# Kernel tuning notes

Measured on AMD Instinct MI355X. Metric: run time of the kernel, lower is better.

## Reference

```python
import jax, jax.numpy as jnp
import numpy as np

N_NODES = 100000
N_EDGES = 3200000
D_IN = 128
D_OUT = 128


def setup_inputs() -> dict:
    key = jax.random.key(0)
    k1, k2, k3 = jax.random.split(key, 3)
    x = jax.random.normal(k1, (N_NODES, D_IN), dtype=jnp.float32)
    edge_index = jax.random.randint(k2, (2, N_EDGES), 0, N_NODES, dtype=jnp.int64)
    # Glorot-style init for GCN weight
    W = jax.random.normal(k3, (D_IN, D_OUT), dtype=jnp.float32) * (1.0 / np.sqrt(D_IN))
    b = jnp.zeros((D_OUT,), dtype=jnp.float32)
    return {"x": x, "edge_index": edge_index, "W": W, "b": b}


def reference(x, edge_index, W, b):
    # GCNConv (PyG semantics): add self-loops, symmetric normalization
    # D^-1/2 A D^-1/2, linear transform, aggregate, add bias; then ReLU.
    N = x.shape[0]
    loops = jnp.arange(N, dtype=edge_index.dtype)
    row = jnp.concatenate([edge_index[0], loops])  # source nodes
    col = jnp.concatenate([edge_index[1], loops])  # target nodes
    # degree over targets, with self-loop weight 1
    deg = jax.ops.segment_sum(jnp.ones_like(col, dtype=x.dtype), col,
                              num_segments=N)
    dinv = jnp.where(deg > 0, 1.0 / jnp.sqrt(deg), 0.0)
    norm = dinv[row] * dinv[col]                   # [E+N]
    xl = x @ W                                     # [N, D_OUT] dense GEMM
    msgs = xl[row] * norm[:, None]                 # gather + scale  [E+N, D_OUT]
    agg = jax.ops.segment_sum(msgs, col, num_segments=N)  # scatter-add
    return jax.nn.relu(agg + b)
```

## Files before the change

### kernel.cpp

```cpp
#include <hip/hip_runtime.h>
#include <hip/hip_bf16.h>
#include <math.h>

#define DF 128
#define TILE_EDGES 6144
#define NPB 128
#define BSH 7
#define NB_MAX 1024
#define KP 136
#define CAP 4864

typedef __hip_bfloat16 bf16;
typedef __attribute__((ext_vector_type(8))) short short8;
typedef __attribute__((ext_vector_type(4))) float f32x4;

__device__ inline short bf16bits(float f) {
    __hip_bfloat16 h = __float2bfloat16(f);
    return *reinterpret_cast<short*>(&h);
}

__device__ inline float4 unpack4(float2 p) {
    unsigned u0 = __float_as_uint(p.x), u1 = __float_as_uint(p.y);
    float4 r;
    r.x = __uint_as_float(u0 << 16);
    r.y = __uint_as_float(u0 & 0xffff0000u);
    r.z = __uint_as_float(u1 << 16);
    r.w = __uint_as_float(u1 & 0xffff0000u);
    return r;
}

__global__ __launch_bounds__(512) void k_binc(const int* __restrict__ col,
                                              int* __restrict__ counts,
                                              int E, int T, int NB) {
    __shared__ int h[NB_MAX];
    int tid = threadIdx.x;
    for (int i = tid; i < NB; i += 512) h[i] = 0;
    __syncthreads();
    int tileBase = blockIdx.x * TILE_EDGES;
    for (int j = 0; j < TILE_EDGES / 512; ++j) {
        int e = tileBase + j * 512 + tid;
        if (e < E) atomicAdd(&h[col[e] >> BSH], 1);
    }
    __syncthreads();
    for (int b = tid; b < NB; b += 512)
        counts[b * T + blockIdx.x] = h[b];
}

__global__ __launch_bounds__(256) void k_scanA(int* __restrict__ data,
                                               int* __restrict__ blockSums, int M) {
    __shared__ int tmp[256];
    int tid = threadIdx.x;
    int n = blockIdx.x * 256 + tid;
    int v = (n < M) ? data[n] : 0;
    tmp[tid] = v;
    __syncthreads();
    for (int off = 1; off < 256; off <<= 1) {
        int t = (tid >= off) ? tmp[tid - off] : 0;
        __syncthreads();
        tmp[tid] += t;
        __syncthreads();
    }
    if (tid == 255) blockSums[blockIdx.x] = tmp[255];
    if (n < M) data[n] = tmp[tid] - v;
}

__global__ __launch_bounds__(1024) void k_scanB(int* __restrict__ blockSums, int nb) {
    __shared__ int tmp[1024];
    int tid = threadIdx.x;
    int carry = 0;
    for (int c0 = 0; c0 < nb; c0 += 1024) {
        int n = c0 + tid;
        int v = (n < nb) ? blockSums[n] : 0;
        tmp[tid] = v;
        __syncthreads();
        for (int off = 1; off < 1024; off <<= 1) {
            int t = (tid >= off) ? tmp[tid - off] : 0;
            __syncthreads();
            tmp[tid] += t;
            __syncthreads();
        }
        if (n < nb) blockSums[n] = carry + tmp[tid] - v;
        carry += tmp[1023];
        __syncthreads();
    }
}

__global__ __launch_bounds__(256) void k_scanC(int* __restrict__ data,
                                               const int* __restrict__ blockSums,
                                               int* __restrict__ bucketBase,
                                               int M, int T, int NB, int E) {
    int n = blockIdx.x * 256 + threadIdx.x;
    if (n >= M) return;
    int v = data[n] + blockSums[n >> 8];
    data[n] = v;
    if (n % T == 0) bucketBase[n / T] = v;
    if (n == 0) bucketBase[NB] = E;
}

__global__ __launch_bounds__(512) void k_binscatter(const int* __restrict__ edge,
                                                    const int* __restrict__ tileOff,
                                                    unsigned* __restrict__ binned,
                                                    int E, int T, int NB) {
    __shared__ int cur[NB_MAX];
    int tid = threadIdx.x;
    int t = blockIdx.x;
    for (int b = tid; b < NB; b += 512) cur[b] = tileOff[b * T + t];
    __syncthreads();
    int tileBase = t * TILE_EDGES;
    for (int j = 0; j < TILE_EDGES / 512; ++j) {
        int e = tileBase + j * 512 + tid;
        if (e < E) {
            int r = edge[e];
            int c = edge[E + e];
            int pos = atomicAdd(&cur[c >> BSH], 1);
            binned[pos] = ((unsigned)(c & (NPB - 1)) << 24) | (unsigned)r;
        }
    }
}

__global__ __launch_bounds__(512) void k_deg(const unsigned* __restrict__ binned,
                                             const int* __restrict__ bucketBase,
                                             int* __restrict__ deg,
                                             float* __restrict__ dinv, int N) {
    __shared__ int h[NPB];
    int tid = threadIdx.x;
    int b = blockIdx.x;
    if (tid < NPB) h[tid] = 0;
    __syncthreads();
    int base = bucketBase[b];
    int cnt = bucketBase[b + 1] - base;
    for (int i = tid; i < cnt; i += 512)
        atomicAdd(&h[binned[base + i] >> 24], 1);
    __syncthreads();
    int node = b * NPB + tid;
    if (tid < NPB && node < N) {
        deg[node] = h[tid];
        dinv[node] = rsqrtf((float)(h[tid] + 1));
    }
}

__global__ __launch_bounds__(256) void k_gemm(const float* __restrict__ x,
                                              const float* __restrict__ W,
                                              const float* __restrict__ dinv,
                                              bf16* __restrict__ y, int N) {
    __shared__ bf16 Wt[DF * KP];
    int tid = threadIdx.x;
    for (int i = tid; i < DF * (DF / 4); i += 256) {
        int k = i >> 5;
        int n4 = (i & 31) * 4;
        float4 w = *(const float4*)(W + k * DF + n4);
        Wt[(n4 + 0) * KP + k] = __float2bfloat16(w.x);
        Wt[(n4 + 1) * KP + k] = __float2bfloat16(w.y);
        Wt[(n4 + 2) * KP + k] = __float2bfloat16(w.z);
        Wt[(n4 + 3) * KP + k] = __float2bfloat16(w.w);
    }
    __syncthreads();

    const int wv = tid >> 6;
    const int lane = tid & 63;
    const int m16 = lane & 15;
    const int q = lane >> 4;
    const int rbase = blockIdx.x * 64 + wv * 16;
    const int arow = min(rbase + m16, N - 1);

    f32x4 acc[8];
#pragma unroll
    for (int nt = 0; nt < 8; ++nt) acc[nt] = (f32x4){0.f, 0.f, 0.f, 0.f};

#pragma unroll
    for (int kc = 0; kc < 4; ++kc) {
        int k0 = kc * 32 + q * 8;
        float4 xa = *(const float4*)(x + (size_t)arow * DF + k0);
        float4 xb = *(const float4*)(x + (size_t)arow * DF + k0 + 4);
        short8 a;
        a[0] = bf16bits(xa.x); a[1] = bf16bits(xa.y);
        a[2] = bf16bits(xa.z); a[3] = bf16bits(xa.w);
        a[4] = bf16bits(xb.x); a[5] = bf16bits(xb.y);
        a[6] = bf16bits(xb.z); a[7] = bf16bits(xb.w);
#pragma unroll
        for (int nt = 0; nt < 8; ++nt) {
            short8 b = *(const short8*)(Wt + (nt * 16 + m16) * KP + k0);
            acc[nt] = __builtin_amdgcn_mfma_f32_16x16x32_bf16(a, b, acc[nt], 0, 0, 0);
        }
    }

#pragma unroll
    for (int r = 0; r < 4; ++r) {
        int orow = rbase + q * 4 + r;
        if (orow < N) {
            float dv = dinv[orow];
#pragma unroll
            for (int nt = 0; nt < 8; ++nt) {
                y[(size_t)orow * DF + nt * 16 + m16] = __float2bfloat16(acc[nt][r] * dv);
            }
        }
    }
}

__global__ __launch_bounds__(512) void k_gatherfused(
        const float* __restrict__ yf,
        const unsigned* __restrict__ binned,
        const int* __restrict__ bucketBase,
        const int* __restrict__ deg,
        const float* __restrict__ bvec,
        int* __restrict__ ssrcG,
        float* __restrict__ out, int N) {
    __shared__ int h[NPB], sc[NPB], cur[NPB];
    __shared__ int lst[CAP];
    int tid = threadIdx.x;
    int b = blockIdx.x;
    int base = bucketBase[b];
    int cnt = bucketBase[b + 1] - base;
    int nodeBase = b * NPB;

    if (tid < NPB) {
        int node = nodeBase + tid;
        int d = (node < N) ? deg[node] : 0;
        h[tid] = d;
        sc[tid] = d;
    }
    __syncthreads();
    for (int off = 1; off < NPB; off <<= 1) {
        int tv = (tid >= off && tid < NPB) ? sc[tid - off] : 0;
        __syncthreads();
        if (tid < NPB) sc[tid] += tv;
        __syncthreads();
    }
    if (tid < NPB) cur[tid] = sc[tid] - h[tid];
    __syncthreads();

    const bool inLds = (cnt <= CAP);
    const int* idxp = inLds ? (const int*)lst : (ssrcG + base);
    for (int i = tid; i < cnt; i += 512) {
        unsigned v = binned[base + i];
        int pos = atomicAdd(&cur[v >> 24], 1);
        int r = (int)(v & 0xFFFFFFu);
        if (inLds) lst[pos] = r; else ssrcG[base + pos] = r;
    }
    __syncthreads();

    int lane = tid & 63;
    int wv = tid >> 6;
    int half = lane >> 5;
    int l32 = lane & 31;

    for (int t = wv; t < NPB; t += 8) {
        int c = nodeBase + t;
        if (c >= N) break;
        int d = h[t];
        int ls = sc[t] - d;

        float4 acc = make_float4(0.f, 0.f, 0.f, 0.f);
        if (half == 0) {
            float2 sv = *(const float2*)(yf + (size_t)c * 64 + l32 * 2);
            acc = unpack4(sv);
        }

        int j = 0;
        for (; j + 16 <= d; j += 16) {
            int r0 = idxp[ls + j + 0 + half];
            int r1 = idxp[ls + j + 2 + half];
            int r2 = idxp[ls + j + 4 + half];
            int r3 = idxp[ls + j + 6 + half];
            int r4 = idxp[ls + j + 8 + half];
            int r5 = idxp[ls + j + 10 + half];
            int r6 = idxp[ls + j + 12 + half];
            int r7 = idxp[ls + j + 14 + half];
            float2 v0 = *(const float2*)(yf + (size_t)r0 * 64 + l32 * 2);
            float2 v1 = *(const float2*)(yf + (size_t)r1 * 64 + l32 * 2);
            float2 v2 = *(const float2*)(yf + (size_t)r2 * 64 + l32 * 2);
            float2 v3 = *(const float2*)(yf + (size_t)r3 * 64 + l32 * 2);
            float2 v4 = *(const float2*)(yf + (size_t)r4 * 64 + l32 * 2);
            float2 v5 = *(const float2*)(yf + (size_t)r5 * 64 + l32 * 2);
            float2 v6 = *(const float2*)(yf + (size_t)r6 * 64 + l32 * 2);
            float2 v7 = *(const float2*)(yf + (size_t)r7 * 64 + l32 * 2);
            float4 u0 = unpack4(v0), u1 = unpack4(v1), u2 = unpack4(v2), u3 = unpack4(v3);
            float4 u4 = unpack4(v4), u5 = unpack4(v5), u6 = unpack4(v6), u7 = unpack4(v7);
            acc.x += ((u0.x + u1.x) + (u2.x + u3.x)) + ((u4.x + u5.x) + (u6.x + u7.x));
            acc.y += ((u0.y + u1.y) + (u2.y + u3.y)) + ((u4.y + u5.y) + (u6.y + u7.y));
            acc.z += ((u0.z + u1.z) + (u2.z + u3.z)) + ((u4.z + u5.z) + (u6.z + u7.z));
            acc.w += ((u0.w + u1.w) + (u2.w + u3.w)) + ((u4.w + u5.w) + (u6.w + u7.w));
        }
        for (; j + 2 <= d; j += 2) {
            int r = idxp[ls + j + half];
            float2 v = *(const float2*)(yf + (size_t)r * 64 + l32 * 2);
            float4 u = unpack4(v);
            acc.x += u.x; acc.y += u.y; acc.z += u.z; acc.w += u.w;
        }
        if (j < d) {
            if (half == 0) {
                int r = idxp[ls + j];
                float2 v = *(const float2*)(yf + (size_t)r * 64 + l32 * 2);
                float4 u = unpack4(v);
                acc.x += u.x; acc.y += u.y; acc.z += u.z; acc.w += u.w;
            }
        }

        acc.x += __shfl_xor(acc.x, 32);
        acc.y += __shfl_xor(acc.y, 32);
        acc.z += __shfl_xor(acc.z, 32);
        acc.w += __shfl_xor(acc.w, 32);

        if (half == 0) {
            float dv = rsqrtf((float)(d + 1));
            float4 bb = *(const float4*)(bvec + l32 * 4);
            float4 o;
            o.x = fmaxf(fmaf(dv, acc.x, bb.x), 0.0f);
            o.y = fmaxf(fmaf(dv, acc.y, bb.y), 0.0f);
            o.z = fmaxf(fmaf(dv, acc.z, bb.z), 0.0f);
            o.w = fmaxf(fmaf(dv, acc.w, bb.w), 0.0f);
            *(float4*)(out + (size_t)c * DF + l32 * 4) = o;
        }
    }
}

extern "C" void kernel_launch(void* const* d_in, const int* in_sizes, int n_in,
                              void* d_out, int out_size, void* d_ws, size_t ws_size,
                              hipStream_t stream) {
    const float* x    = (const float*)d_in[0];
    const int*   edge = (const int*)d_in[1];
    const float* W    = (const float*)d_in[2];
    const float* b    = (const float*)d_in[3];
    float*       out  = (float*)d_out;

    const int N = in_sizes[0] / DF;
    const int E = in_sizes[1] / 2;

    const int T  = (E + TILE_EDGES - 1) / TILE_EDGES;
    const int NB = (N + NPB - 1) / NPB;
    const int M  = NB * T;

    bf16*     y          = (bf16*)d_ws;
    int*      deg        = (int*)(y + (size_t)N * DF);
    float*    dinv       = (float*)(deg + N);
    int*      bucketBase = (int*)(dinv + N);
    int*      blockSums  = bucketBase + NB_MAX + 8;
    int*      counts     = blockSums + 2048;
    unsigned* binned     = (unsigned*)(counts + M);
    int*      ssrc       = (int*)(binned + E);

    const int nbM = (M + 255) / 256;

    k_binc<<<T, 512, 0, stream>>>(edge + E, counts, E, T, NB);
    k_scanA<<<nbM, 256, 0, stream>>>(counts, blockSums, M);
    k_scanB<<<1, 1024, 0, stream>>>(blockSums, nbM);
    k_scanC<<<nbM, 256, 0, stream>>>(counts, blockSums, bucketBase, M, T, NB, E);
    k_binscatter<<<T, 512, 0, stream>>>(edge, counts, binned, E, T, NB);
    k_deg<<<NB, 512, 0, stream>>>(binned, bucketBase, deg, dinv, N);
    k_gemm<<<(N + 63) / 64, 256, 0, stream>>>(x, W, dinv, y, N);
    k_gatherfused<<<NB, 512, 0, stream>>>((const float*)y, binned, bucketBase, deg,
                                          b, ssrc, out, N);
}
```

Before: 339.6 us.

## Split CSR build from gather; one wave per node with shuffled indices

The per-bucket sort into source lists moves from the gather kernel into the degree kernel, which now writes a global CSR (offsets plus sorted sources). The gather becomes a standalone kernel with one wave per destination node and small blocks, loading 64 indices per wave and broadcasting them with shuffles. The aim is better load balance and occupancy, since the LDS list buffer and the serialized per-block node loop are gone. The cost is an extra global write and read of the sorted index array, and the edge tile size is halved, with counts aliased onto ssrc.

```diff
diff --git a/kernel.cpp b/kernel.cpp
--- a/kernel.cpp
+++ b/kernel.cpp
@@ -3,12 +3,11 @@
 #include <math.h>
 
 #define DF 128
-#define TILE_EDGES 6144
+#define TILE_EDGES 3072
 #define NPB 128
 #define BSH 7
 #define NB_MAX 1024
 #define KP 136
-#define CAP 4864
 
 typedef __hip_bfloat16 bf16;
 typedef __attribute__((ext_vector_type(8))) short short8;
@@ -118,24 +117,45 @@
     }
 }
 
-__global__ __launch_bounds__(512) void k_deg(const unsigned* __restrict__ binned,
-                                             const int* __restrict__ bucketBase,
-                                             int* __restrict__ deg,
-                                             float* __restrict__ dinv, int N) {
-    __shared__ int h[NPB];
+__global__ __launch_bounds__(512) void k_bucket(const unsigned* __restrict__ binned,
+                                                const int* __restrict__ bucketBase,
+                                                int* __restrict__ ssrc,
+                                                int* __restrict__ offsets,
+                                                int* __restrict__ deg,
+                                                float* __restrict__ dinv, int N) {
+    __shared__ int h[NPB], sc[NPB], cur[NPB];
     int tid = threadIdx.x;
     int b = blockIdx.x;
-    if (tid < NPB) h[tid] = 0;
-    __syncthreads();
     int base = bucketBase[b];
     int cnt = bucketBase[b + 1] - base;
+    if (tid < NPB) h[tid] = 0;
+    __syncthreads();
     for (int i = tid; i < cnt; i += 512)
         atomicAdd(&h[binned[base + i] >> 24], 1);
     __syncthreads();
-    int node = b * NPB + tid;
-    if (tid < NPB && node < N) {
-        deg[node] = h[tid];
-        dinv[node] = rsqrtf((float)(h[tid] + 1));
+    if (tid < NPB) sc[tid] = h[tid];
+    __syncthreads();
+    for (int off = 1; off < NPB; off <<= 1) {
+        int tv = (tid >= off && tid < NPB) ? sc[tid - off] : 0;
+        __syncthreads();
+        if (tid < NPB) sc[tid] += tv;
+        __syncthreads();
+    }
+    if (tid < NPB) {
+        int excl = sc[tid] - h[tid];
+        cur[tid] = base + excl;
+        int node = b * NPB + tid;
+        if (node < N) {
+            offsets[node] = base + excl;
+            deg[node] = h[tid];
+            dinv[node] = rsqrtf((float)(h[tid] + 1));
+        }
+    }
+    __syncthreads();
+    for (int i = tid; i < cnt; i += 512) {
+        unsigned v = binned[base + i];
+        int pos = atomicAdd(&cur[v >> 24], 1);
+        ssrc[pos] = (int)(v & 0xFFFFFFu);
     }
 }
 
@@ -197,75 +217,41 @@
     }
 }
 
-__global__ __launch_bounds__(512) void k_gatherfused(
-        const float* __restrict__ yf,
-        const unsigned* __restrict__ binned,
-        const int* __restrict__ bucketBase,
-        const int* __restrict__ deg,
-        const float* __restrict__ bvec,
-        int* __restrict__ ssrcG,
-        float* __restrict__ out, int N) {
-    __shared__ int h[NPB], sc[NPB], cur[NPB];
-    __shared__ int lst[CAP];
-    int tid = threadIdx.x;
-    int b = blockIdx.x;
-    int base = bucketBase[b];
-    int cnt = bucketBase[b + 1] - base;
-    int nodeBase = b * NPB;
-
-    if (tid < NPB) {
-        int node = nodeBase + tid;
-        int d = (node < N) ? deg[node] : 0;
-        h[tid] = d;
-        sc[tid] = d;
-    }
-    __syncthreads();
-    for (int off = 1; off < NPB; off <<= 1) {
-        int tv = (tid >= off && tid < NPB) ? sc[tid - off] : 0;
-        __syncthreads();
-        if (tid < NPB) sc[tid] += tv;
-        __syncthreads();
-    }
-    if (tid < NPB) cur[tid] = sc[tid] - h[tid];
-    __syncthreads();
-
-    const bool inLds = (cnt <= CAP);
-    const int* idxp = inLds ? (const int*)lst : (ssrcG + base);
-    for (int i = tid; i < cnt; i += 512) {
-        unsigned v = binned[base + i];
-        int pos = atomicAdd(&cur[v >> 24], 1);
-        int r = (int)(v & 0xFFFFFFu);
-        if (inLds) lst[pos] = r; else ssrcG[base + pos] = r;
-    }
-    __syncthreads();
-
-    int lane = tid & 63;
-    int wv = tid >> 6;
+__global__ __launch_bounds__(256) void k_gather(const float* __restrict__ yf,
+                                                const int* __restrict__ ssrc,
+                                                const int* __restrict__ offsets,
+                                                const int* __restrict__ deg,
+                                                const float* __restrict__ dinv,
+                                                const float* __restrict__ bvec,
+                                                float* __restrict__ out, int N) {
+    int wave = (blockIdx.x * 256 + threadIdx.x) >> 6;
+    int lane = threadIdx.x & 63;
+    if (wave >= N) return;
+    int c = wave;
+    int start = offsets[c];
+    int d = deg[c];
     int half = lane >> 5;
     int l32 = lane & 31;
 
-    for (int t = wv; t < NPB; t += 8) {
-        int c = nodeBase + t;
-        if (c >= N) break;
-        int d = h[t];
-        int ls = sc[t] - d;
-
-        float4 acc = make_float4(0.f, 0.f, 0.f, 0.f);
-        if (half == 0) {
-            float2 sv = *(const float2*)(yf + (size_t)c * 64 + l32 * 2);
-            acc = unpack4(sv);
-        }
-
+    float4 acc = make_float4(0.f, 0.f, 0.f, 0.f);
+    if (half == 0) {
+        float2 sv = *(const float2*)(yf + (size_t)c * 64 + l32 * 2);
+        acc = unpack4(sv);
+    }
+
+    for (int base = 0; base < d; base += 64) {
+        int nb = min(64, d - base);
+        int idx = ssrc[start + base + min(lane, nb - 1)];
         int j = 0;
-        for (; j + 16 <= d; j += 16) {
-            int r0 = idxp[ls + j + 0 + half];
-            int r1 = idxp[ls + j + 2 + half];
-            int r2 = idxp[ls + j + 4 + half];
-            int r3 = idxp[ls + j + 6 + half];
-            int r4 = idxp[ls + j + 8 + half];
-            int r5 = idxp[ls + j + 10 + half];
-            int r6 = idxp[ls + j + 12 + half];
-            int r7 = idxp[ls + j + 14 + half];
+        for (; j + 16 <= nb; j += 16) {
+            int r0 = __shfl(idx, j + 0 + half);
+            int r1 = __shfl(idx, j + 2 + half);
+            int r2 = __shfl(idx, j + 4 + half);
+            int r3 = __shfl(idx, j + 6 + half);
+            int r4 = __shfl(idx, j + 8 + half);
+            int r5 = __shfl(idx, j + 10 + half);
+            int r6 = __shfl(idx, j + 12 + half);
+            int r7 = __shfl(idx, j + 14 + half);
             float2 v0 = *(const float2*)(yf + (size_t)r0 * 64 + l32 * 2);
             float2 v1 = *(const float2*)(yf + (size_t)r1 * 64 + l32 * 2);
             float2 v2 = *(const float2*)(yf + (size_t)r2 * 64 + l32 * 2);
@@ -281,36 +267,36 @@
             acc.z += ((u0.z + u1.z) + (u2.z + u3.z)) + ((u4.z + u5.z) + (u6.z + u7.z));
             acc.w += ((u0.w + u1.w) + (u2.w + u3.w)) + ((u4.w + u5.w) + (u6.w + u7.w));
         }
-        for (; j + 2 <= d; j += 2) {
-            int r = idxp[ls + j + half];
+        for (; j + 2 <= nb; j += 2) {
+            int r = __shfl(idx, j + half);
             float2 v = *(const float2*)(yf + (size_t)r * 64 + l32 * 2);
             float4 u = unpack4(v);
             acc.x += u.x; acc.y += u.y; acc.z += u.z; acc.w += u.w;
         }
-        if (j < d) {
+        if (j < nb) {
+            int r = __shfl(idx, j);
             if (half == 0) {
-                int r = idxp[ls + j];
                 float2 v = *(const float2*)(yf + (size_t)r * 64 + l32 * 2);
                 float4 u = unpack4(v);
                 acc.x += u.x; acc.y += u.y; acc.z += u.z; acc.w += u.w;
             }
         }
-
-        acc.x += __shfl_xor(acc.x, 32);
-        acc.y += __shfl_xor(acc.y, 32);
-        acc.z += __shfl_xor(acc.z, 32);
-        acc.w += __shfl_xor(acc.w, 32);
-
-        if (half == 0) {
-            float dv = rsqrtf((float)(d + 1));
-            float4 bb = *(const float4*)(bvec + l32 * 4);
-            float4 o;
-            o.x = fmaxf(fmaf(dv, acc.x, bb.x), 0.0f);
-            o.y = fmaxf(fmaf(dv, acc.y, bb.y), 0.0f);
-            o.z = fmaxf(fmaf(dv, acc.z, bb.z), 0.0f);
-            o.w = fmaxf(fmaf(dv, acc.w, bb.w), 0.0f);
-            *(float4*)(out + (size_t)c * DF + l32 * 4) = o;
-        }
+    }
+
+    acc.x += __shfl_xor(acc.x, 32);
+    acc.y += __shfl_xor(acc.y, 32);
+    acc.z += __shfl_xor(acc.z, 32);
+    acc.w += __shfl_xor(acc.w, 32);
+
+    if (half == 0) {
+        float dv = dinv[c];
+        float4 bb = *(const float4*)(bvec + l32 * 4);
+        float4 o;
+        o.x = fmaxf(fmaf(dv, acc.x, bb.x), 0.0f);
+        o.y = fmaxf(fmaf(dv, acc.y, bb.y), 0.0f);
+        o.z = fmaxf(fmaf(dv, acc.z, bb.z), 0.0f);
+        o.w = fmaxf(fmaf(dv, acc.w, bb.w), 0.0f);
+        *(float4*)(out + (size_t)c * DF + l32 * 4) = o;
     }
 }
 
@@ -333,11 +319,12 @@
     bf16*     y          = (bf16*)d_ws;
     int*      deg        = (int*)(y + (size_t)N * DF);
     float*    dinv       = (float*)(deg + N);
-    int*      bucketBase = (int*)(dinv + N);
+    int*      offsets    = (int*)(dinv + N);
+    int*      bucketBase = offsets + N + 8;
     int*      blockSums  = bucketBase + NB_MAX + 8;
-    int*      counts     = blockSums + 2048;
-    unsigned* binned     = (unsigned*)(counts + M);
-    int*      ssrc       = (int*)(binned + E);
+    int*      ssrc       = blockSums + 4096;
+    int*      counts     = ssrc;
+    unsigned* binned     = (unsigned*)(ssrc + E);
 
     const int nbM = (M + 255) / 256;
 
@@ -346,8 +333,7 @@
     k_scanB<<<1, 1024, 0, stream>>>(blockSums, nbM);
     k_scanC<<<nbM, 256, 0, stream>>>(counts, blockSums, bucketBase, M, T, NB, E);
     k_binscatter<<<T, 512, 0, stream>>>(edge, counts, binned, E, T, NB);
-    k_deg<<<NB, 512, 0, stream>>>(binned, bucketBase, deg, dinv, N);
+    k_bucket<<<NB, 512, 0, stream>>>(binned, bucketBase, ssrc, offsets, deg, dinv, N);
     k_gemm<<<(N + 63) / 64, 256, 0, stream>>>(x, W, dinv, y, N);
-    k_gatherfused<<<NB, 512, 0, stream>>>((const float*)y, binned, bucketBase, deg,
-                                          b, ssrc, out, N);
-}
+    k_gather<<<(N + 3) / 4, 256, 0, stream>>>((const float*)y, ssrc, offsets, deg, dinv, b, out, N);
+}
```

After: 337.3 us. Within noise of the previous version (-0.7%).
